# Optimization experiments

Measured on AMD Instinct MI355X. Metric: run time of the kernel, lower is better.

Reference implementation:

```python
import jax, jax.numpy as jnp
import numpy as np

NEG_SLOPE = 0.2


def setup_inputs() -> dict:
    key = jax.random.key(0)
    k1, k2, k3, k4, k5, k6 = jax.random.split(key, 6)
    N, E, IN, OUT = 100000, 1600000, 256, 32
    feat = jax.random.normal(k1, (N, IN), dtype=jnp.float32)
    W = jax.random.normal(k2, (IN, OUT), dtype=jnp.float32) * (1.0 / np.sqrt(IN))
    attn_l = jax.random.normal(k3, (OUT,), dtype=jnp.float32) * 0.1
    attn_r = jax.random.normal(k4, (OUT,), dtype=jnp.float32) * 0.1
    bias = jnp.zeros((OUT,), dtype=jnp.float32)
    src = jax.random.randint(k5, (E,), 0, N, dtype=jnp.int32)
    dst = jax.random.randint(k6, (E,), 0, N, dtype=jnp.int32)
    return {"feat": feat, "W": W, "attn_l": attn_l, "attn_r": attn_r,
            "bias": bias, "src": src, "dst": dst}


def reference(feat, W, attn_l, attn_r, bias, src, dst):
    N = feat.shape[0]
    # dense projection: [N, in] @ [in, out] -> [N, out]
    h = feat @ W
    el = h @ attn_l  # [N]
    er = h @ attn_r  # [N]
    # per-edge raw score: el[u] + er[v] for edge u->v
    e = el[src] + er[dst]  # [E]
    e = jnp.where(e > 0, e, NEG_SLOPE * e)  # leaky relu
    # edge softmax grouped by destination node (numerically stable)
    m = jax.ops.segment_max(e, dst, num_segments=N)  # [N], -inf for isolated nodes
    m = jax.lax.stop_gradient(m)
    ex = jnp.exp(e - m[dst])  # [E]
    denom = jax.ops.segment_sum(ex, dst, num_segments=N)  # [N]
    alpha = ex / denom[dst]  # [E]
    # weighted aggregation (sparse SpMM): sum_{u->v} alpha_uv * h[u]
    rst = jax.ops.segment_sum(h[src] * alpha[:, None], dst, num_segments=N)  # [N, out]
    return rst + bias
```

## Files before the change

### kernel.cpp

```cpp
#include <hip/hip_runtime.h>
#include <hip/hip_bf16.h>
#include <math.h>

#define NEG_SLOPE 0.2f

#define CBITS 8
#define CNODES 256
#define CAPC 4672
#define NC_MAX 400
#define NBIN 256
#define NGEMM 256

typedef __bf16 bf16x8 __attribute__((ext_vector_type(8)));
typedef __bf16 bf16x4 __attribute__((ext_vector_type(4)));
typedef float  f32x4  __attribute__((ext_vector_type(4)));

__global__ void prep(const float* __restrict__ W, __bf16* __restrict__ Whi,
                     unsigned int* __restrict__ ccur) {
    int idx = blockIdx.x * blockDim.x + threadIdx.x;
    if (idx < NC_MAX) ccur[idx] = 0u;
    if (idx >= 8192) return;
    int j = idx & 7, lane = (idx >> 3) & 63, nt = (idx >> 9) & 1, kt = idx >> 10;
    int q = lane >> 4, c = lane & 15;
    int k = kt * 32 + q * 8 + j;
    int n = nt * 16 + c;
    Whi[idx] = (__bf16)W[k * 32 + n];
}

__global__ __launch_bounds__(256) void gemm_bin(const float* __restrict__ feat,
                                                const __bf16* __restrict__ Whi,
                                                const float* __restrict__ attn_l,
                                                const float* __restrict__ attn_r,
                                                const int* __restrict__ src,
                                                const int* __restrict__ dst,
                                                __bf16* __restrict__ hb,
                                                float* __restrict__ el,
                                                float* __restrict__ er,
                                                unsigned int* __restrict__ ccur,
                                                unsigned int* __restrict__ cbin,
                                                int N, int Ntiles, int E, int NC) {
    union SM {
        struct { bf16x8 whi[1024]; float stage[4][2][1024]; } g;
        struct { unsigned int hist[NC_MAX]; unsigned int cbase[NC_MAX]; } b;
    };
    __shared__ SM sm;

    int bid = blockIdx.x;
    int tid = threadIdx.x;
    int role = bid & 1, gid = bid >> 1;

    if (role == 1) {
        unsigned int* hist  = sm.b.hist;
        unsigned int* cbase = sm.b.cbase;
        int batch = (((E + NBIN - 1) / NBIN) + 3) & ~3;
        int b0 = gid * batch;
        int b1 = min(b0 + batch, E);
        int nv = (b0 < b1) ? ((b1 - b0) >> 2) : 0;
        const int4* d4 = (const int4*)(dst + b0);
        const int4* s4 = (const int4*)(src + b0);
        for (int i = tid; i < NC; i += 256) hist[i] = 0;
        __syncthreads();
        for (int i = tid; i < nv; i += 256) {
            int4 dd = d4[i];
#pragma unroll
            for (int j = 0; j < 4; j++)
                atomicAdd(&hist[((unsigned)(&dd.x)[j]) >> CBITS], 1u);
        }
        __syncthreads();
        for (int i = tid; i < NC; i += 256) {
            unsigned c = hist[i];
            cbase[i] = c ? atomicAdd(&ccur[i], c) : 0u;
            hist[i] = 0;
        }
        __syncthreads();
        for (int i = tid; i < nv; i += 256) {
            int4 dd = d4[i];
            int4 ss = s4[i];
#pragma unroll
            for (int j = 0; j < 4; j++) {
                int d = (&dd.x)[j];
                int s = (&ss.x)[j];
                unsigned cb = ((unsigned)d) >> CBITS;
                unsigned r = atomicAdd(&hist[cb], 1u);
                unsigned pos = cbase[cb] + r;
                if (pos < CAPC)
                    cbin[(size_t)cb * CAPC + pos] =
                        ((unsigned)(d & (CNODES - 1)) << 17) | (unsigned)s;
            }
        }
        return;
    }

    for (int i = tid; i < 1024; i += 256) sm.g.whi[i] = ((const bf16x8*)Whi)[i];
    __syncthreads();

    int wv   = tid >> 6;
    int lane = tid & 63;
    int cc = lane & 15, qd = lane >> 4;
    int swz = (cc & 7) << 4;

    int gw = gid * 4 + wv;
    int nt = (Ntiles - gw + 1023) >> 10;
    int Q  = 4 * nt;

    float* buf0 = &sm.g.stage[wv][0][0];
    float* buf1 = &sm.g.stage[wv][1][0];

    auto stage_q = [&](int q) {
        int qc = q < Q ? q : Q - 1;
        int t  = gw + ((qc >> 2) << 10);
        int kq = qc & 3;
        float* lb = (q & 1) ? buf1 : buf0;
#pragma unroll
        for (int j = 0; j < 4; j++) {
            int r = 4 * j + (lane >> 4);
            int grow = t * 16 + r;
            if (grow >= N) grow = N - 1;
            int seg = ((lane & 15) * 16) ^ ((r & 7) << 4);
            const char* sp = (const char*)feat +
                             ((size_t)grow * 256 + kq * 64) * 4 + seg;
            __builtin_amdgcn_global_load_lds(
                (const __attribute__((address_space(1))) void*)sp,
                (__attribute__((address_space(3))) void*)(lb + j * 256),
                16, 0, 0);
        }
    };

    stage_q(0);
    stage_q(1);

    float alc  = attn_l[cc],      arc  = attn_r[cc];
    float alc2 = attn_l[cc + 16], arc2 = attn_r[cc + 16];

    f32x4 acc0 = {0.f, 0.f, 0.f, 0.f};
    f32x4 acc1 = {0.f, 0.f, 0.f, 0.f};

    for (int i = 0; i < nt; i++) {
#pragma unroll
        for (int kq2 = 0; kq2 < 4; kq2++) {
            int q = i * 4 + kq2;
            asm volatile("s_waitcnt vmcnt(4)" ::: "memory");
            __builtin_amdgcn_sched_barrier(0);
            const char* lb = (const char*)((q & 1) ? buf1 : buf0);
#pragma unroll
            for (int jj = 0; jj < 2; jj++) {
                int kt = kq2 * 2 + jj;
                int so = jj * 128 + qd * 32;
                f32x4 a0 = *(const f32x4*)(lb + cc * 256 + ((so)      ^ swz));
                f32x4 a1 = *(const f32x4*)(lb + cc * 256 + ((so + 16) ^ swz));
                bf16x8 ah, al;
#pragma unroll
                for (int j = 0; j < 4; j++) {
                    __bf16 h0 = (__bf16)a0[j];
                    __bf16 h1 = (__bf16)a1[j];
                    ah[j]     = h0;
                    ah[j + 4] = h1;
                    al[j]     = (__bf16)(a0[j] - (float)h0);
                    al[j + 4] = (__bf16)(a1[j] - (float)h1);
                }
                bf16x8 bh0 = sm.g.whi[(kt * 2 + 0) * 64 + lane];
                bf16x8 bh1 = sm.g.whi[(kt * 2 + 1) * 64 + lane];
                acc0 = __builtin_amdgcn_mfma_f32_16x16x32_bf16(ah, bh0, acc0, 0, 0, 0);
                acc0 = __builtin_amdgcn_mfma_f32_16x16x32_bf16(al, bh0, acc0, 0, 0, 0);
                acc1 = __builtin_amdgcn_mfma_f32_16x16x32_bf16(ah, bh1, acc1, 0, 0, 0);
                acc1 = __builtin_amdgcn_mfma_f32_16x16x32_bf16(al, bh1, acc1, 0, 0, 0);
            }
            if (kq2 == 3) {
                int t = gw + (i << 10);
#pragma unroll
                for (int r = 0; r < 4; r++) {
                    int m = t * 16 + qd * 4 + r;
                    if (m < N) {
                        hb[(size_t)m * 32 + cc]      = (__bf16)acc0[r];
                        hb[(size_t)m * 32 + 16 + cc] = (__bf16)acc1[r];
                    }
                    float pl = acc0[r] * alc + acc1[r] * alc2;
                    float pr = acc0[r] * arc + acc1[r] * arc2;
#pragma unroll
                    for (int off = 8; off >= 1; off >>= 1) {
                        pl += __shfl_xor(pl, off);
                        pr += __shfl_xor(pr, off);
                    }
                    if (cc == 0 && m < N) { el[m] = pl; er[m] = pr; }
                }
                acc0 = (f32x4){0.f, 0.f, 0.f, 0.f};
                acc1 = (f32x4){0.f, 0.f, 0.f, 0.f};
            }
            __builtin_amdgcn_sched_barrier(0);
            stage_q(q + 2);
        }
    }
}

__global__ __launch_bounds__(512) void aggregate(const unsigned int* __restrict__ ccur,
                                                 const unsigned int* __restrict__ cbin,
                                                 const float* __restrict__ el,
                                                 const float* __restrict__ er,
                                                 const __bf16* __restrict__ hb,
                                                 const float* __restrict__ bias,
                                                 float* __restrict__ out, int N) {
    __shared__ uint2        rw_s[CAPC];
    __shared__ unsigned int hist[CNODES];
    __shared__ int          off_s[CNODES + 1];
    __shared__ float        den[CNODES];
    __shared__ float        er_l[CNODES];
    __shared__ int          wsum[5];

    int cb = blockIdx.x;
    int base = cb << CBITS;
    int nn = min(CNODES, N - base);
    int tid = threadIdx.x;
    int lane = tid & 63, wvv = tid >> 6;

    int cnt = (int)min(ccur[cb], (unsigned)CAPC);
    const unsigned int* cp = cbin + (size_t)cb * CAPC;

    if (tid < CNODES) {
        hist[tid] = 0;
        den[tid] = 0.f;
        er_l[tid] = (tid < nn) ? er[base + tid] : 0.f;
    }
    __syncthreads();

    for (int i = tid; i < cnt; i += 512)
        atomicAdd(&hist[(cp[i] >> 17) & (CNODES - 1)], 1u);
    __syncthreads();

    int v = 0, orig = 0;
    if (tid < CNODES) {
        v = (int)hist[tid];
        orig = v;
#pragma unroll
        for (int off = 1; off < 64; off <<= 1) {
            int x = __shfl_up(v, off, 64);
            if (lane >= off) v += x;
        }
        if (lane == 63) wsum[wvv] = v;
    }
    __syncthreads();
    if (tid == 0) {
        int s = 0;
#pragma unroll
        for (int w = 0; w < 4; w++) { int t = wsum[w]; wsum[w] = s; s += t; }
        wsum[4] = s;
    }
    __syncthreads();
    if (tid < CNODES) {
        int off = v - orig + wsum[wvv];
        off_s[tid] = off;
        hist[tid] = (unsigned)off;
        if (tid == CNODES - 1) off_s[CNODES] = wsum[4];
    }
    __syncthreads();

    for (int i = tid; i < cnt; i += 512) {
        unsigned r = cp[i];
        int s  = (int)(r & 0x1FFFFu);
        int ln = (int)((r >> 17) & (CNODES - 1));
        float e = el[s] + er_l[ln];
        e = (e > 0.f) ? e : NEG_SLOPE * e;
        float w = __expf(e);
        unsigned pos = atomicAdd(&hist[ln], 1u);
        if (pos < CAPC) {
            rw_s[pos] = make_uint2((unsigned)s, __float_as_uint(w));
            atomicAdd(&den[ln], w);
        }
    }
    __syncthreads();

    int oct = lane >> 3, t = lane & 7;
    f32x4 b4 = *(const f32x4*)&bias[t * 4];
    for (int n = wvv; n < nn; n += 8) {
        float sm = den[n];
        int s0 = off_s[n], s1 = off_s[n + 1];
        f32x4 acc = {0.f, 0.f, 0.f, 0.f};
#pragma unroll 2
        for (int j = s0 + oct; j < s1; j += 8) {
            uint2 rw = rw_s[j];
            float w = __uint_as_float(rw.y);
            bf16x4 hv = *(const bf16x4*)&hb[(size_t)rw.x * 32 + t * 4];
            acc[0] += w * (float)hv[0];
            acc[1] += w * (float)hv[1];
            acc[2] += w * (float)hv[2];
            acc[3] += w * (float)hv[3];
        }
#pragma unroll
        for (int off = 8; off <= 32; off <<= 1) {
            acc[0] += __shfl_xor(acc[0], off);
            acc[1] += __shfl_xor(acc[1], off);
            acc[2] += __shfl_xor(acc[2], off);
            acc[3] += __shfl_xor(acc[3], off);
        }
        if (lane < 8) {
            f32x4 o;
            if (sm > 0.f) {
                float inv = 1.f / sm;
                o[0] = acc[0] * inv + b4[0];
                o[1] = acc[1] * inv + b4[1];
                o[2] = acc[2] * inv + b4[2];
                o[3] = acc[3] * inv + b4[3];
            } else {
                o = b4;
            }
            *(f32x4*)&out[(size_t)(base + n) * 32 + t * 4] = o;
        }
    }
}

static inline size_t align256(size_t x) { return (x + 255) & ~(size_t)255; }

extern "C" void kernel_launch(void* const* d_in, const int* in_sizes, int n_in,
                              void* d_out, int out_size, void* d_ws, size_t ws_size,
                              hipStream_t stream) {
    const float* feat   = (const float*)d_in[0];
    const float* W      = (const float*)d_in[1];
    const float* attn_l = (const float*)d_in[2];
    const float* attn_r = (const float*)d_in[3];
    const float* bias   = (const float*)d_in[4];
    const int* src = (const int*)d_in[5];
    const int* dst = (const int*)d_in[6];
    float* out = (float*)d_out;

    const int IN = 256;
    int N = in_sizes[0] / IN;
    int E = in_sizes[5];
    (void)n_in; (void)out_size; (void)ws_size;

    int Ntiles = (N + 15) / 16;
    int NC   = (N + CNODES - 1) >> CBITS;

    char* p = (char*)d_ws;
    __bf16* hb     = (__bf16*)p; p += align256((size_t)N * 32 * 2);
    float* el      = (float*)p; p += align256((size_t)N * 4);
    float* er      = (float*)p; p += align256((size_t)N * 4);
    unsigned int* ccur = (unsigned int*)p; p += align256((size_t)NC_MAX * 4);
    unsigned int* cbin = (unsigned int*)p; p += align256((size_t)NC * CAPC * 4);
    __bf16* Whi    = (__bf16*)p; p += align256((size_t)8192 * 2);

    prep<<<33, 256, 0, stream>>>(W, Whi, ccur);
    gemm_bin<<<NGEMM + NBIN, 256, 0, stream>>>(feat, Whi, attn_l, attn_r,
                                               src, dst, hb, el, er, ccur, cbin,
                                               N, Ntiles, E, NC);
    aggregate<<<NC, 512, 0, stream>>>(ccur, cbin, el, er, hb, bias, out, N);
}
```

Measured before the change: 233.7 us.

## Split aggregate into sort kernel and finer-grained gather kernel over 32-node buckets

The fused aggregate kernel is split in two. A sort kernel computes edge weights, buckets them by destination into a global buffer, and writes per-node offsets and softmax denominators. A second kernel then runs the weighted gather with 256-thread blocks over 32-node buckets, so there are many more blocks and no large shared-memory footprint, which should raise occupancy and balance load across CUs. In exchange it adds a kernel launch and writes and re-reads the sorted edge list through global memory instead of LDS.

```diff
diff --git a/kernel.cpp b/kernel.cpp
--- a/kernel.cpp
+++ b/kernel.cpp
@@ -3,6 +3,8 @@
 #include <math.h>
 
 #define NEG_SLOPE 0.2f
+#define BUCK_BITS 5
+#define BUCK_NODES 32
 
 #define CBITS 8
 #define CNODES 256
@@ -192,23 +194,21 @@
     }
 }
 
-__global__ __launch_bounds__(512) void aggregate(const unsigned int* __restrict__ ccur,
-                                                 const unsigned int* __restrict__ cbin,
-                                                 const float* __restrict__ el,
-                                                 const float* __restrict__ er,
-                                                 const __bf16* __restrict__ hb,
-                                                 const float* __restrict__ bias,
-                                                 float* __restrict__ out, int N) {
-    __shared__ uint2        rw_s[CAPC];
+__global__ __launch_bounds__(512) void sortw(const unsigned int* __restrict__ ccur,
+                                             const unsigned int* __restrict__ cbin,
+                                             const float* __restrict__ el,
+                                             const float* __restrict__ er,
+                                             uint2* __restrict__ fbin,
+                                             int* __restrict__ noff,
+                                             float* __restrict__ deng,
+                                             int N, int NC) {
     __shared__ unsigned int hist[CNODES];
-    __shared__ int          off_s[CNODES + 1];
-    __shared__ float        den[CNODES];
+    __shared__ float        denL[CNODES];
     __shared__ float        er_l[CNODES];
     __shared__ int          wsum[5];
 
     int cb = blockIdx.x;
     int base = cb << CBITS;
-    int nn = min(CNODES, N - base);
     int tid = threadIdx.x;
     int lane = tid & 63, wvv = tid >> 6;
 
@@ -217,8 +217,8 @@
 
     if (tid < CNODES) {
         hist[tid] = 0;
-        den[tid] = 0.f;
-        er_l[tid] = (tid < nn) ? er[base + tid] : 0.f;
+        denL[tid] = 0.f;
+        er_l[tid] = (base + tid < N) ? er[base + tid] : 0.f;
     }
     __syncthreads();
 
@@ -247,9 +247,9 @@
     __syncthreads();
     if (tid < CNODES) {
         int off = v - orig + wsum[wvv];
-        off_s[tid] = off;
+        noff[cb * 257 + tid] = cb * CAPC + off;
         hist[tid] = (unsigned)off;
-        if (tid == CNODES - 1) off_s[CNODES] = wsum[4];
+        if (tid == 0) noff[cb * 257 + CNODES] = cb * CAPC + cnt;
     }
     __syncthreads();
 
@@ -261,22 +261,41 @@
         e = (e > 0.f) ? e : NEG_SLOPE * e;
         float w = __expf(e);
         unsigned pos = atomicAdd(&hist[ln], 1u);
-        if (pos < CAPC) {
-            rw_s[pos] = make_uint2((unsigned)s, __float_as_uint(w));
-            atomicAdd(&den[ln], w);
-        }
-    }
-    __syncthreads();
-
+        if (pos < (unsigned)CAPC) {
+            fbin[(size_t)cb * CAPC + pos] =
+                make_uint2((unsigned)s, __float_as_uint(w));
+            atomicAdd(&denL[ln], w);
+        }
+    }
+    __syncthreads();
+    if (tid < CNODES && base + tid < N) deng[base + tid] = denL[tid];
+}
+
+__global__ __launch_bounds__(256) void aggregate(const int* __restrict__ noff,
+                                                 const float* __restrict__ deng,
+                                                 const uint2* __restrict__ fbin,
+                                                 const __bf16* __restrict__ hb,
+                                                 const float* __restrict__ bias,
+                                                 float* __restrict__ out, int N) {
+    int buck = blockIdx.x;
+    int cb = buck >> 3;
+    int fo = (buck & 7) << 5;
+    int base = buck << BUCK_BITS;
+    int nn = min(BUCK_NODES, N - base);
+    int tid = threadIdx.x;
+    int lane = tid & 63, wv = tid >> 6;
     int oct = lane >> 3, t = lane & 7;
+
+    const int* np = noff + cb * 257 + fo;
     f32x4 b4 = *(const f32x4*)&bias[t * 4];
-    for (int n = wvv; n < nn; n += 8) {
-        float sm = den[n];
-        int s0 = off_s[n], s1 = off_s[n + 1];
+
+    for (int n = wv; n < nn; n += 4) {
+        int s0 = np[n], s1 = np[n + 1];
+        float sm = deng[base + n];
         f32x4 acc = {0.f, 0.f, 0.f, 0.f};
 #pragma unroll 2
         for (int j = s0 + oct; j < s1; j += 8) {
-            uint2 rw = rw_s[j];
+            uint2 rw = fbin[j];
             float w = __uint_as_float(rw.y);
             bf16x4 hv = *(const bf16x4*)&hb[(size_t)rw.x * 32 + t * 4];
             acc[0] += w * (float)hv[0];
@@ -327,19 +346,24 @@
     (void)n_in; (void)out_size; (void)ws_size;
 
     int Ntiles = (N + 15) / 16;
+    int NBUK = (N + BUCK_NODES - 1) >> BUCK_BITS;
     int NC   = (N + CNODES - 1) >> CBITS;
 
     char* p = (char*)d_ws;
     __bf16* hb     = (__bf16*)p; p += align256((size_t)N * 32 * 2);
     float* el      = (float*)p; p += align256((size_t)N * 4);
     float* er      = (float*)p; p += align256((size_t)N * 4);
+    float* deng    = (float*)p; p += align256((size_t)N * 4);
     unsigned int* ccur = (unsigned int*)p; p += align256((size_t)NC_MAX * 4);
     unsigned int* cbin = (unsigned int*)p; p += align256((size_t)NC * CAPC * 4);
+    uint2* fbin    = (uint2*)p; p += align256((size_t)NC * CAPC * 8);
+    int* noff      = (int*)p;   p += align256((size_t)NC_MAX * 257 * 4);
     __bf16* Whi    = (__bf16*)p; p += align256((size_t)8192 * 2);
 
     prep<<<33, 256, 0, stream>>>(W, Whi, ccur);
     gemm_bin<<<NGEMM + NBIN, 256, 0, stream>>>(feat, Whi, attn_l, attn_r,
                                                src, dst, hb, el, er, ccur, cbin,
                                                N, Ntiles, E, NC);
-    aggregate<<<NC, 512, 0, stream>>>(ccur, cbin, el, er, hb, bias, out, N);
-}
+    sortw<<<NC, 512, 0, stream>>>(ccur, cbin, el, er, fbin, noff, deng, N, NC);
+    aggregate<<<NBUK, 256, 0, stream>>>(noff, deng, fbin, hb, bias, out, N);
+}
```

Result: slower. 241.4 us (+3.3%).
